# Optimization experiments

Hardware: AMD Instinct MI355X
Metric: run time of the kernel (lower is better)

## Reference

```python
import jax, jax.numpy as jnp
import numpy as np

D_MIN, D_MAX, D_COUNT = 0.0, 6.0, 16
HIDDEN = 128
N_NODES, N_EDGES = 50000, 1600000


def _rbf(D):
    # D: [E] -> [E, D_COUNT]
    mu = jnp.linspace(D_MIN, D_MAX, D_COUNT, dtype=D.dtype)  # [16]
    sigma = (D_MAX - D_MIN) / D_COUNT
    return jnp.exp(-(((D[:, None] - mu[None, :]) / sigma) ** 2))


def setup_inputs() -> dict:
    key = jax.random.key(0)
    k1, k2, k3, k4 = jax.random.split(key, 4)
    pos = jax.random.normal(k1, (N_NODES, 3), dtype=jnp.float32) * 3.0
    edge_index = jax.random.randint(k2, (2, N_EDGES), 0, N_NODES, dtype=jnp.int64)
    # Linear(16, hidden): PyTorch default init U(-1/sqrt(16), 1/sqrt(16))
    bound = 1.0 / np.sqrt(D_COUNT)
    W = jax.random.uniform(k3, (D_COUNT, HIDDEN), jnp.float32, -bound, bound)
    b = jax.random.uniform(k4, (HIDDEN,), jnp.float32, -bound, bound)
    return {"pos": pos, "edge_index": edge_index, "W": W, "b": b}


def reference(pos, edge_index, W, b):
    # gather endpoints: [E, 3]
    coord_diff = pos[edge_index[0]] - pos[edge_index[1]]
    dist = jnp.linalg.norm(coord_diff, axis=1)        # [E]
    rbf = _rbf(dist)                                  # [E, 16]
    return jax.nn.sigmoid(rbf @ W + b)                # [E, hidden]
```

## Files before the change

### kernel.cpp

```cpp
#include <hip/hip_runtime.h>
#include <math.h>

#define N_NODES 50000
#define N_EDGES 1600000
#define HIDDEN  128
#define DC      16
#define EPB     64
#define BLOCK   256

#define MU_STEP   0.4f
#define INV_SIGMA 2.6666666666666665f

__device__ __forceinline__ float fast_sigmoid(float x) {
    float e = __expf(-x);
    return __builtin_amdgcn_rcpf(1.0f + e);
}

__global__ __launch_bounds__(BLOCK, 4) void edge_attr_kernel(
    const float* __restrict__ pos,
    const int* __restrict__ ei,
    const float* __restrict__ W,
    const float* __restrict__ b,
    float* __restrict__ out)
{
    __shared__ float rbf_s[DC][EPB];

    const int tid = threadIdx.x;
    const int h4  = tid & 31;
    const int eo  = tid >> 5;

    float4 wcol[DC];
    #pragma unroll
    for (int k = 0; k < DC; ++k)
        wcol[k] = *reinterpret_cast<const float4*>(W + k * HIDDEN + h4 * 4);
    const float4 bias = *reinterpret_cast<const float4*>(b + h4 * 4);

    {
        const int el = tid & 63;
        const int kg = tid >> 6;
        const int e = blockIdx.x * EPB + el;
        const int s = ei[e];
        const int d = ei[N_EDGES + e];
        const float dx = pos[3 * s + 0] - pos[3 * d + 0];
        const float dy = pos[3 * s + 1] - pos[3 * d + 1];
        const float dz = pos[3 * s + 2] - pos[3 * d + 2];
        const float dist = sqrtf(dx * dx + dy * dy + dz * dz);
        #pragma unroll
        for (int j = 0; j < 4; ++j) {
            const int k = kg * 4 + j;
            const float t = (dist - MU_STEP * (float)k) * INV_SIGMA;
            rbf_s[k][el] = __expf(-t * t);
        }
    }
    __syncthreads();

    const size_t row0 = (size_t)blockIdx.x * EPB;
    #pragma unroll
    for (int i = 0; i < EPB / 8; ++i) {
        const int el = eo + i * 8;

        float r[DC];
        #pragma unroll
        for (int k = 0; k < DC; ++k) r[k] = rbf_s[k][el];

        float4 acc = bias;
        #pragma unroll
        for (int k = 0; k < DC; ++k) {
            acc.x = fmaf(r[k], wcol[k].x, acc.x);
            acc.y = fmaf(r[k], wcol[k].y, acc.y);
            acc.z = fmaf(r[k], wcol[k].z, acc.z);
            acc.w = fmaf(r[k], wcol[k].w, acc.w);
        }
        acc.x = fast_sigmoid(acc.x);
        acc.y = fast_sigmoid(acc.y);
        acc.z = fast_sigmoid(acc.z);
        acc.w = fast_sigmoid(acc.w);

        *reinterpret_cast<float4*>(out + (row0 + el) * HIDDEN + h4 * 4) = acc;
    }
}

extern "C" void kernel_launch(void* const* d_in, const int* in_sizes, int n_in,
                              void* d_out, int out_size, void* d_ws, size_t ws_size,
                              hipStream_t stream) {
    const float* pos = (const float*)d_in[0];
    const int*   ei  = (const int*)d_in[1];
    const float* W   = (const float*)d_in[2];
    const float* b   = (const float*)d_in[3];
    float*       out = (float*)d_out;

    dim3 grid(N_EDGES / EPB);
    edge_attr_kernel<<<grid, BLOCK, 0, stream>>>(pos, ei, W, b, out);
}
```

Baseline: 865.6 us.

## Restructure edge kernel: per-edge distance, row-major RBF smem, nontemporal 2-wide stores

Computes each edge's distance once into shared memory, then fills a padded row-major RBF buffer so each edge's 16 basis values are read as vector loads. It also doubles edges per block, switches each thread to two hidden outputs, writes with nontemporal stores, and raises the occupancy hint. The aim is to cut redundant gather/sqrt work and LDS traffic and to speed up the write-bound output stream. The vector pos load reads one float past the last node.

Result: faster. 824.3 us (-4.8%).

```diff
diff --git a/kernel.cpp b/kernel.cpp
--- a/kernel.cpp
+++ b/kernel.cpp
@@ -5,78 +5,118 @@
 #define N_EDGES 1600000
 #define HIDDEN  128
 #define DC      16
-#define EPB     64
+#define EPB     128
 #define BLOCK   256
+#define RBF_LD  20
 
 #define MU_STEP   0.4f
 #define INV_SIGMA 2.6666666666666665f
+
+typedef float f32x2 __attribute__((ext_vector_type(2)));
+typedef float f32x4 __attribute__((ext_vector_type(4)));
+typedef f32x4 f32x4u __attribute__((aligned(4)));
 
 __device__ __forceinline__ float fast_sigmoid(float x) {
     float e = __expf(-x);
     return __builtin_amdgcn_rcpf(1.0f + e);
 }
 
-__global__ __launch_bounds__(BLOCK, 4) void edge_attr_kernel(
+__device__ __forceinline__ f32x2 fma2(float s, f32x2 w, f32x2 a) {
+    a.x = fmaf(s, w.x, a.x);
+    a.y = fmaf(s, w.y, a.y);
+    return a;
+}
+
+__global__ __launch_bounds__(BLOCK, 6) void edge_attr_kernel(
     const float* __restrict__ pos,
     const int* __restrict__ ei,
     const float* __restrict__ W,
     const float* __restrict__ b,
     float* __restrict__ out)
 {
-    __shared__ float rbf_s[DC][EPB];
+    __shared__ float dist_s[EPB];
+    __shared__ float rbf_s[EPB][RBF_LD];
 
     const int tid = threadIdx.x;
-    const int h4  = tid & 31;
-    const int eo  = tid >> 5;
+    const int h2  = tid & 63;
+    const int wv  = tid >> 6;
 
-    float4 wcol[DC];
+    f32x2 wcol[DC];
     #pragma unroll
     for (int k = 0; k < DC; ++k)
-        wcol[k] = *reinterpret_cast<const float4*>(W + k * HIDDEN + h4 * 4);
-    const float4 bias = *reinterpret_cast<const float4*>(b + h4 * 4);
+        wcol[k] = *reinterpret_cast<const f32x2*>(W + k * HIDDEN + h2 * 2);
+    const f32x2 bias = *reinterpret_cast<const f32x2*>(b + h2 * 2);
 
-    {
-        const int el = tid & 63;
-        const int kg = tid >> 6;
-        const int e = blockIdx.x * EPB + el;
+    const long row0 = (long)blockIdx.x * EPB;
+
+    if (tid < EPB) {
+        const int e = (int)row0 + tid;
         const int s = ei[e];
         const int d = ei[N_EDGES + e];
-        const float dx = pos[3 * s + 0] - pos[3 * d + 0];
-        const float dy = pos[3 * s + 1] - pos[3 * d + 1];
-        const float dz = pos[3 * s + 2] - pos[3 * d + 2];
-        const float dist = sqrtf(dx * dx + dy * dy + dz * dz);
-        #pragma unroll
-        for (int j = 0; j < 4; ++j) {
-            const int k = kg * 4 + j;
-            const float t = (dist - MU_STEP * (float)k) * INV_SIGMA;
-            rbf_s[k][el] = __expf(-t * t);
-        }
+        const f32x4 ps = *reinterpret_cast<const f32x4u*>(pos + 3 * s);
+        const f32x4 pd = *reinterpret_cast<const f32x4u*>(pos + 3 * d);
+        const float dx = ps.x - pd.x;
+        const float dy = ps.y - pd.y;
+        const float dz = ps.z - pd.z;
+        dist_s[tid] = sqrtf(dx * dx + dy * dy + dz * dz);
     }
     __syncthreads();
 
-    const size_t row0 = (size_t)blockIdx.x * EPB;
-    #pragma unroll
-    for (int i = 0; i < EPB / 8; ++i) {
-        const int el = eo + i * 8;
+    {
+        const int el = tid & 127;
+        const int kg = tid >> 7;
+        const float dist = dist_s[el];
+        f32x4 r0, r1;
+        #pragma unroll
+        for (int j = 0; j < 4; ++j) {
+            const float t = (dist - MU_STEP * (float)(kg * 8 + j)) * INV_SIGMA;
+            r0[j] = __expf(-t * t);
+        }
+        #pragma unroll
+        for (int j = 0; j < 4; ++j) {
+            const float t = (dist - MU_STEP * (float)(kg * 8 + 4 + j)) * INV_SIGMA;
+            r1[j] = __expf(-t * t);
+        }
+        *reinterpret_cast<f32x4*>(&rbf_s[el][kg * 8 + 0]) = r0;
+        *reinterpret_cast<f32x4*>(&rbf_s[el][kg * 8 + 4]) = r1;
+    }
+    __syncthreads();
 
-        float r[DC];
-        #pragma unroll
-        for (int k = 0; k < DC; ++k) r[k] = rbf_s[k][el];
+    float* op = out + (row0 + wv) * HIDDEN + h2 * 2;
+    #pragma unroll 4
+    for (int i = 0; i < EPB / 4; ++i) {
+        const int el = wv + i * 4;
 
-        float4 acc = bias;
-        #pragma unroll
-        for (int k = 0; k < DC; ++k) {
-            acc.x = fmaf(r[k], wcol[k].x, acc.x);
-            acc.y = fmaf(r[k], wcol[k].y, acc.y);
-            acc.z = fmaf(r[k], wcol[k].z, acc.z);
-            acc.w = fmaf(r[k], wcol[k].w, acc.w);
-        }
-        acc.x = fast_sigmoid(acc.x);
-        acc.y = fast_sigmoid(acc.y);
-        acc.z = fast_sigmoid(acc.z);
-        acc.w = fast_sigmoid(acc.w);
+        const f32x4* rp = reinterpret_cast<const f32x4*>(&rbf_s[el][0]);
+        const f32x4 ra = rp[0];
+        const f32x4 rb = rp[1];
+        const f32x4 rc = rp[2];
+        const f32x4 rd = rp[3];
 
-        *reinterpret_cast<float4*>(out + (row0 + el) * HIDDEN + h4 * 4) = acc;
+        f32x2 acc = bias;
+        acc = fma2(ra.x, wcol[0],  acc);
+        acc = fma2(ra.y, wcol[1],  acc);
+        acc = fma2(ra.z, wcol[2],  acc);
+        acc = fma2(ra.w, wcol[3],  acc);
+        acc = fma2(rb.x, wcol[4],  acc);
+        acc = fma2(rb.y, wcol[5],  acc);
+        acc = fma2(rb.z, wcol[6],  acc);
+        acc = fma2(rb.w, wcol[7],  acc);
+        acc = fma2(rc.x, wcol[8],  acc);
+        acc = fma2(rc.y, wcol[9],  acc);
+        acc = fma2(rc.z, wcol[10], acc);
+        acc = fma2(rc.w, wcol[11], acc);
+        acc = fma2(rd.x, wcol[12], acc);
+        acc = fma2(rd.y, wcol[13], acc);
+        acc = fma2(rd.z, wcol[14], acc);
+        acc = fma2(rd.w, wcol[15], acc);
+
+        f32x2 res;
+        res.x = fast_sigmoid(acc.x);
+        res.y = fast_sigmoid(acc.y);
+
+        __builtin_nontemporal_store(res, reinterpret_cast<f32x2*>(op));
+        op += 4 * HIDDEN;
     }
 }
 
```
